# Kernel optimization log

Hardware: AMD Instinct MI355X
Metric: run time of the kernel (lower is better)

## Reference

```python
import jax, jax.numpy as jnp
import numpy as np

B, N, D, H = 4, 2048, 1024, 16
HD = D // H          # head dim before LRPE doubling
CHUNK = 64
BASE = 10000.0
EPS = 1e-6


def setup_inputs() -> dict:
    key = jax.random.key(0)
    ks = jax.random.split(key, 8)
    s = 0.02
    return {
        "x": jax.random.normal(ks[0], (B, N, D), jnp.float32),
        "Wq": jax.random.normal(ks[1], (D, D), jnp.float32) * s,
        "Wk": jax.random.normal(ks[2], (D, D), jnp.float32) * s,
        "Wv": jax.random.normal(ks[3], (D, D), jnp.float32) * s,
        "Wo": jax.random.normal(ks[4], (D, D), jnp.float32) * s,
        "Wg1": jax.random.normal(ks[5], (D, H), jnp.float32) * s,
        "Wg2": jax.random.normal(ks[6], (H, D), jnp.float32) * s,
        "norm_w": jnp.ones((D,), jnp.float32),
    }


def _lrpe(x, theta):
    # cosine LRPE (lrpe_type=6): d -> 2d, concat([x*cos, x*sin])
    c = jnp.cos(theta)[None, :, None, :]
    s = jnp.sin(theta)[None, :, None, :]
    return jnp.concatenate([x * c, x * s], axis=-1)


def _chunk_gla(q, k, v, g):
    # GLA chunked scan: S_t = diag(exp(g_t)) S_{t-1} + k_t^T v_t ; o_t = q_t S_t
    # q,k,g: (b,n,h,dk), v: (b,n,h,dv)
    b, n, h, dk = q.shape
    dv = v.shape[-1]
    nc = n // CHUNK

    def to_chunks(t):
        return t.reshape(b, nc, CHUNK, t.shape[2], t.shape[3]).transpose(1, 0, 2, 3, 4)

    qc, kc, vc, gc = map(to_chunks, (q, k, v, g))  # (nc,b,C,h,*)
    mask = jnp.tril(jnp.ones((CHUNK, CHUNK), bool))

    def step(S, inp):
        qi, ki, vi, gi = inp                      # (b,C,h,dk/dv)
        G = jnp.cumsum(gi, axis=1)                # inclusive cumsum of log decay
        q_g = qi * jnp.exp(G)
        k_g = ki * jnp.exp(-G)
        o_inter = jnp.einsum('bchk,bhkv->bchv', q_g, S)
        A = jnp.einsum('bchk,bshk->bhcs', q_g, k_g)
        A = jnp.where(mask[None, None], A, 0.0)
        o_intra = jnp.einsum('bhcs,bshv->bchv', A, vi)
        G_last = G[:, -1:]                        # (b,1,h,dk)
        S = S * jnp.exp(G_last[:, 0])[..., None] + jnp.einsum(
            'bchk,bchv->bhkv', ki * jnp.exp(G_last - G), vi)
        return S, o_inter + o_intra

    S0 = jnp.zeros((b, h, dk, dv), q.dtype)
    _, o = jax.lax.scan(step, S0, (qc, kc, vc, gc))
    return o.transpose(1, 0, 2, 3, 4).reshape(b, n, h, dv)


def reference(x, Wq, Wk, Wv, Wo, Wg1, Wg2, norm_w):
    b, n, d = x.shape
    q = jax.nn.silu(x @ Wq).reshape(b, n, H, HD)
    k_raw = (x @ Wk).reshape(b, n, H, HD)
    v = (x @ Wv).reshape(b, n, H, HD)

    # log-space cumulative decay from raw k projection (scalar_decay=False path)
    f = jnp.concatenate([jnp.zeros((b, 1, H, HD), jnp.float32),
                         k_raw.astype(jnp.float32)], axis=1)
    z = jax.lax.cumlogsumexp(f, axis=1)           # (b,n+1,H,HD)
    log_f = z[:, :-1] - z[:, 1:]                  # per-step log decay (<=0)
    k = jnp.exp(k_raw - z[:, 1:])                 # normalized keys

    # cosine LRPE: angles (n,HD), doubles head dim
    theta = jnp.arange(n, dtype=jnp.float32)[:, None] * \
        (BASE ** (-2.0 * jnp.arange(HD, dtype=jnp.float32) / HD))[None]
    q = _lrpe(q, theta)
    k = _lrpe(k, theta)
    g = jnp.concatenate([log_f, log_f], axis=-1)  # repeat '... d -> ... (2 d)'

    o = _chunk_gla(q, k, v, g)                    # (b,n,H,HD)
    o = o.reshape(b, n, d)

    gate = jax.nn.sigmoid((x @ Wg1) @ Wg2)        # low-rank output gate
    o = o * gate
    o = o * jax.lax.rsqrt(jnp.mean(o * o, axis=-1, keepdims=True) + EPS) * norm_w
    return o @ Wo
```

## Files before the change

### kernel.cpp

```cpp
#include <hip/hip_runtime.h>
#include <hip/hip_bf16.h>
#include <math.h>

#define B_ 4
#define N_ 2048
#define D_ 1024
#define H_ 16
#define HD_ 64

typedef __attribute__((ext_vector_type(8))) short bf16x8;
typedef __attribute__((ext_vector_type(8))) unsigned short u16x8;
typedef __attribute__((ext_vector_type(4))) float f32x4;

#define AS1(p) ((const __attribute__((address_space(1))) void*)(p))
#define AS3(p) ((__attribute__((address_space(3))) void*)(p))

__device__ inline float bf2f(unsigned short u) { return __uint_as_float(((unsigned)u) << 16); }
__device__ inline unsigned short f2bf(float f) {
  unsigned u = __float_as_uint(f);
  return (unsigned short)((u + 0x7fffu + ((u >> 16) & 1u)) >> 16);
}
__device__ inline unsigned short f2h(float f) {
  _Float16 h = (_Float16)f; unsigned short u; __builtin_memcpy(&u, &h, 2); return u;
}
__device__ inline float h2f(unsigned short u) {
  _Float16 h; __builtin_memcpy(&h, &u, 2); return (float)h;
}
__device__ inline float lseop_fast(float a, float b) {
  float mx = fmaxf(a, b), mn = fminf(a, b);
  return mx + __logf(1.f + __expf(mn - mx));
}

__global__ __launch_bounds__(256) void prep_all(
    const float* __restrict__ x, const float* __restrict__ Wq,
    const float* __restrict__ Wk, const float* __restrict__ Wv,
    const float* __restrict__ Wo, const float* __restrict__ Wg1,
    unsigned short* __restrict__ xb, unsigned short* __restrict__ Wqkv_p,
    unsigned short* __restrict__ Wo_p, unsigned short* __restrict__ Wg1p,
    float* __restrict__ ropeT) {
  const int bid = blockIdx.x;
  if (bid < 4096) {
    const int t = bid * 256 + threadIdx.x;
    float4 a = ((const float4*)x)[(size_t)t * 2];
    float4 b = ((const float4*)x)[(size_t)t * 2 + 1];
    union { unsigned short u[8]; uint4 q; } pk;
    pk.u[0] = f2bf(a.x); pk.u[1] = f2bf(a.y); pk.u[2] = f2bf(a.z); pk.u[3] = f2bf(a.w);
    pk.u[4] = f2bf(b.x); pk.u[5] = f2bf(b.y); pk.u[6] = f2bf(b.z); pk.u[7] = f2bf(b.w);
    ((uint4*)xb)[t] = pk.q;
  } else if (bid < 6144) {
    const int wb = bid - 4096;
    const int which = wb >> 9;
    const float* W = (which == 0) ? Wq : (which == 1) ? Wk : (which == 2) ? Wv : Wo;
    const int col0 = (which == 1) ? 1024 : (which == 2) ? 2048 : 0;
    const int Ntot = (which == 3) ? 1024 : 3072;
    unsigned short* dst = (which == 3) ? Wo_p : Wqkv_p;
    const int t = (wb & 511) * 256 + threadIdx.x;
    const int kg = t >> 10, n = t & 1023;
    union { unsigned short u[8]; uint4 q; } pk;
#pragma unroll
    for (int r = 0; r < 8; ++r)
      pk.u[r] = f2bf(W[(size_t)(kg * 8 + r) * 1024 + n]);
    *(uint4*)&dst[((size_t)kg * Ntot + col0 + n) * 8] = pk.q;
  } else if (bid < 6656) {
    const int t = (bid - 6144) * 256 + threadIdx.x;
    const int n = t >> 6, hd = t & 63;
    const float freq = expf((float)hd * -0.28782313662425575f);
    float s, c;
    sincosf((float)n * freq, &s, &c);
    ropeT[(size_t)n * 128 + hd] = c;
    ropeT[(size_t)n * 128 + 64 + hd] = s;
  } else {
    const int t = (bid - 6656) * 256 + threadIdx.x;
    const int kg = t >> 4, hh = t & 15;
    union { unsigned short us[8]; u16x8 v; } pk;
#pragma unroll
    for (int r = 0; r < 8; ++r)
      pk.us[r] = f2bf(Wg1[(size_t)(kg * 8 + r) * 16 + hh]);
    *(u16x8*)&Wg1p[((size_t)kg * 16 + hh) * 8] = pk.v;
  }
}

__global__ __launch_bounds__(256) void gate_logits(
    const unsigned short* __restrict__ x_bf, const unsigned short* __restrict__ Wg1p,
    float* __restrict__ tg) {
  __shared__ unsigned short Wl[128 * 16 * 8];
  const int tid = threadIdx.x;
  const int lane = tid & 63, w = tid >> 6;
  const int lr = lane & 15, lg = lane >> 4;
#pragma unroll
  for (int u = 0; u < 8; ++u) {
    const int flat = u * 256 + tid;
    *(u16x8*)&Wl[flat * 8] = *(const u16x8*)&Wg1p[(size_t)flat * 8];
  }
  __syncthreads();
  const int row = blockIdx.x * 64 + w * 16 + lr;
  f32x4 acc = (f32x4){0.f, 0.f, 0.f, 0.f};
  for (int ks = 0; ks < 32; ++ks) {
    bf16x8 a = *(const bf16x8*)&x_bf[(size_t)row * 1024 + ks * 32 + lg * 8];
    bf16x8 b = *(const bf16x8*)&Wl[((ks * 4 + lg) * 16 + lr) * 8];
    acc = __builtin_amdgcn_mfma_f32_16x16x32_bf16(a, b, acc, 0, 0, 0);
  }
  const int orow = blockIdx.x * 64 + w * 16 + 4 * lg;
#pragma unroll
  for (int reg = 0; reg < 4; ++reg)
    tg[(size_t)(orow + reg) * 16 + lr] = acc[reg];
}

__global__ __launch_bounds__(256) void gemm_qkv(
    const unsigned short* __restrict__ A, const unsigned short* __restrict__ Wp,
    unsigned short* __restrict__ qb, unsigned short* __restrict__ keh,
    unsigned short* __restrict__ vb, float* __restrict__ T, int M, int K) {
  const int Nn = 3072;
  __shared__ unsigned short Asm[2][128 * 32];
  __shared__ unsigned short Bsm[2][4 * 128 * 8];

  const int tid = threadIdx.x;
  const int lane = tid & 63;
  const int w = tid >> 6;
  const int nwg = gridDim.x;
  const int cpx = nwg >> 3;
  const int orig = blockIdx.x;
  const int L = (orig & 7) * cpx + (orig >> 3);
  const int st = L >> 6;
  const int j = L & 63;
  const int by = (st / 3) * 8 + (j >> 3);
  const int bx = (st % 3) * 8 + (j & 7);
  const int m0 = by * 128, n0 = bx * 128;
  const int wr = w >> 1, wc = w & 1;

  f32x4 acc[4][4];
#pragma unroll
  for (int i = 0; i < 4; ++i)
#pragma unroll
    for (int jj = 0; jj < 4; ++jj) acc[i][jj] = (f32x4){0.f, 0.f, 0.f, 0.f};

  const int rA0 = w * 16 + (lane >> 2);
  const int rA1 = (w + 4) * 16 + (lane >> 2);
  const int sA0 = (lane & 3) ^ ((rA0 >> 1) & 3);
  const int sA1 = (lane & 3) ^ ((rA1 >> 1) & 3);
  const unsigned short* gA0 = A + (size_t)(m0 + rA0) * K + sA0 * 8;
  const unsigned short* gA1 = A + (size_t)(m0 + rA1) * K + sA1 * 8;
  const unsigned short* gB0 = Wp + (size_t)(w >> 1) * Nn * 8 +
                              (size_t)(n0 + (w & 1) * 64 + lane) * 8;
  const unsigned short* gB1 = Wp + (size_t)((w + 4) >> 1) * Nn * 8 +
                              (size_t)(n0 + ((w + 4) & 1) * 64 + lane) * 8;

  int offA[4], offB[4];
#pragma unroll
  for (int m = 0; m < 4; ++m) {
    const int rowf = wr * 64 + m * 16 + (lane & 15);
    const int sp = (lane >> 4) ^ ((rowf >> 1) & 3);
    offA[m] = rowf * 32 + sp * 8;
  }
#pragma unroll
  for (int n = 0; n < 4; ++n) {
    const int colf = wc * 64 + n * 16 + (lane & 15);
    offB[n] = (lane >> 4) * 1024 + colf * 8;
  }

  auto STAGE = [&](int buf, int t) {
    const int kt = t * 32;
    const size_t kB = (size_t)(kt >> 3) * Nn * 8;
    __builtin_amdgcn_global_load_lds(AS1(gA0 + kt), AS3(&Asm[buf][w * 512]), 16, 0, 0);
    __builtin_amdgcn_global_load_lds(AS1(gA1 + kt), AS3(&Asm[buf][(w + 4) * 512]), 16, 0, 0);
    __builtin_amdgcn_global_load_lds(AS1(gB0 + kB), AS3(&Bsm[buf][w * 512]), 16, 0, 0);
    __builtin_amdgcn_global_load_lds(AS1(gB1 + kB), AS3(&Bsm[buf][(w + 4) * 512]), 16, 0, 0);
  };

  const int NT = K >> 5;
  STAGE(0, 0);
  __syncthreads();
  int cur = 0;
  for (int t = 0; t < NT; ++t) {
    if (t + 1 < NT) STAGE(cur ^ 1, t + 1);
    bf16x8 af[4], bfr[4];
#pragma unroll
    for (int m = 0; m < 4; ++m) af[m] = *(const bf16x8*)&Asm[cur][offA[m]];
#pragma unroll
    for (int n = 0; n < 4; ++n) bfr[n] = *(const bf16x8*)&Bsm[cur][offB[n]];
#pragma unroll
    for (int m = 0; m < 4; ++m)
#pragma unroll
      for (int n = 0; n < 4; ++n)
        acc[m][n] = __builtin_amdgcn_mfma_f32_16x16x32_bf16(af[m], bfr[n], acc[m][n], 0, 0, 0);
    __syncthreads();
    cur ^= 1;
  }

  const int crow = (lane >> 4) * 4;
  const int ccol = lane & 15;
  const int slice = bx >> 3;
  if (slice == 1) {
#pragma unroll
    for (int n = 0; n < 4; ++n) {
      float se = 0.f;
#pragma unroll
      for (int m = 0; m < 4; ++m)
#pragma unroll
        for (int r = 0; r < 4; ++r) {
          float ev = __expf(acc[m][n][r]);
          se += ev;
          keh[(size_t)(m0 + wr * 64 + m * 16 + crow + r) * 1024 +
              (n0 & 1023) + wc * 64 + n * 16 + ccol] = f2h(ev);
        }
      se += __shfl_xor(se, 16);
      se += __shfl_xor(se, 32);
      if ((lane >> 4) == 0) {
        const int bb = m0 >> 11;
        const int h = ((n0 & 1023) + wc * 64) >> 6;
        const int hd = n * 16 + ccol;
        const int c = ((m0 & 2047) >> 6) + wr;
        T[(size_t)((bb * 16 + h) * 64 + hd) * 32 + c] = __logf(se);
      }
    }
  } else {
#pragma unroll
    for (int m = 0; m < 4; ++m)
#pragma unroll
      for (int n = 0; n < 4; ++n)
#pragma unroll
        for (int r = 0; r < 4; ++r) {
          float vv = acc[m][n][r];
          const size_t idx = (size_t)(m0 + wr * 64 + m * 16 + crow + r) * 1024 +
                             (n0 & 1023) + wc * 64 + n * 16 + ccol;
          if (slice == 0) {
            vv = vv / (1.f + __expf(-vv));
            qb[idx] = f2bf(vv);
          } else {
            vb[idx] = f2bf(vv);
          }
        }
  }
}

__global__ __launch_bounds__(256) void gemm_bf16(
    const unsigned short* __restrict__ A, const unsigned short* __restrict__ Wp,
    float* __restrict__ Cf, int M, int K, int Nn) {
  __shared__ unsigned short Asm[2][128 * 32];
  __shared__ unsigned short Bsm[2][4 * 128 * 8];

  const int tid = threadIdx.x;
  const int lane = tid & 63;
  const int w = tid >> 6;
  const int nb = Nn >> 7;
  const int nwg = gridDim.x;
  const int cpx = nwg >> 3;
  int bid = blockIdx.x;
  bid = (bid & 7) * cpx + (bid >> 3);
  const int by = bid / nb, bx = bid % nb;
  const int m0 = by * 128, n0 = bx * 128;
  const int wr = w >> 1, wc = w & 1;

  f32x4 acc[4][4];
#pragma unroll
  for (int i = 0; i < 4; ++i)
#pragma unroll
    for (int j = 0; j < 4; ++j) acc[i][j] = (f32x4){0.f, 0.f, 0.f, 0.f};

  const int rA0 = w * 16 + (lane >> 2);
  const int rA1 = (w + 4) * 16 + (lane >> 2);
  const int sA0 = (lane & 3) ^ ((rA0 >> 1) & 3);
  const int sA1 = (lane & 3) ^ ((rA1 >> 1) & 3);
  const unsigned short* gA0 = A + (size_t)(m0 + rA0) * K + sA0 * 8;
  const unsigned short* gA1 = A + (size_t)(m0 + rA1) * K + sA1 * 8;
  const unsigned short* gB0 = Wp + (size_t)(w >> 1) * Nn * 8 +
                              (size_t)(n0 + (w & 1) * 64 + lane) * 8;
  const unsigned short* gB1 = Wp + (size_t)((w + 4) >> 1) * Nn * 8 +
                              (size_t)(n0 + ((w + 4) & 1) * 64 + lane) * 8;

  int offA[4], offB[4];
#pragma unroll
  for (int m = 0; m < 4; ++m) {
    const int rowf = wr * 64 + m * 16 + (lane & 15);
    const int sp = (lane >> 4) ^ ((rowf >> 1) & 3);
    offA[m] = rowf * 32 + sp * 8;
  }
#pragma unroll
  for (int n = 0; n < 4; ++n) {
    const int colf = wc * 64 + n * 16 + (lane & 15);
    offB[n] = (lane >> 4) * 1024 + colf * 8;
  }

  auto STAGE = [&](int buf, int t) {
    const int kt = t * 32;
    const size_t kB = (size_t)(kt >> 3) * Nn * 8;
    __builtin_amdgcn_global_load_lds(AS1(gA0 + kt), AS3(&Asm[buf][w * 512]), 16, 0, 0);
    __builtin_amdgcn_global_load_lds(AS1(gA1 + kt), AS3(&Asm[buf][(w + 4) * 512]), 16, 0, 0);
    __builtin_amdgcn_global_load_lds(AS1(gB0 + kB), AS3(&Bsm[buf][w * 512]), 16, 0, 0);
    __builtin_amdgcn_global_load_lds(AS1(gB1 + kB), AS3(&Bsm[buf][(w + 4) * 512]), 16, 0, 0);
  };

  const int NT = K >> 5;
  STAGE(0, 0);
  __syncthreads();
  int cur = 0;
  for (int t = 0; t < NT; ++t) {
    if (t + 1 < NT) STAGE(cur ^ 1, t + 1);
    bf16x8 af[4], bfr[4];
#pragma unroll
    for (int m = 0; m < 4; ++m) af[m] = *(const bf16x8*)&Asm[cur][offA[m]];
#pragma unroll
    for (int n = 0; n < 4; ++n) bfr[n] = *(const bf16x8*)&Bsm[cur][offB[n]];
#pragma unroll
    for (int m = 0; m < 4; ++m)
#pragma unroll
      for (int n = 0; n < 4; ++n)
        acc[m][n] = __builtin_amdgcn_mfma_f32_16x16x32_bf16(af[m], bfr[n], acc[m][n], 0, 0, 0);
    __syncthreads();
    cur ^= 1;
  }

  const int crow = (lane >> 4) * 4;
  const int ccol = lane & 15;
#pragma unroll
  for (int m = 0; m < 4; ++m)
#pragma unroll
    for (int n = 0; n < 4; ++n) {
#pragma unroll
      for (int r = 0; r < 4; ++r) {
        Cf[(size_t)(m0 + wr * 64 + m * 16 + crow + r) * Nn +
           n0 + wc * 64 + n * 16 + ccol] = acc[m][n][r];
      }
    }
}

__global__ void scan_pass_b(const float* __restrict__ T, float* __restrict__ Pf) {
  const int ch = blockIdx.x * 256 + threadIdx.x;
  const float* t = &T[(size_t)ch * 32];
  float* p = &Pf[(size_t)ch * 32];
  float run = 0.f;
  for (int c = 0; c < 32; ++c) {
    p[c] = run;
    run = lseop_fast(run, t[c]);
  }
}

__global__ __launch_bounds__(256) void gla_a(
    const unsigned short* __restrict__ qs, const unsigned short* __restrict__ keh,
    const float* __restrict__ Pf, const unsigned short* __restrict__ v_bf,
    const float* __restrict__ ropeT,
    unsigned short* __restrict__ qg_p, unsigned short* __restrict__ U,
    unsigned short* __restrict__ o_bf, float* __restrict__ glast_g) {
  __shared__ unsigned short kg_l[64 * 128];
  __shared__ unsigned short kgT_l[128 * 72];
  __shared__ unsigned short vT_l[64 * 72];
  __shared__ unsigned short G_l[64 * 72];
  __shared__ unsigned short tot_l[4][64];
  __shared__ float glast_s[64];
  unsigned short* A_l = G_l;

  const int bid = blockIdx.x;
  const int bh = bid >> 5, c = bid & 31;
  const int b = bh >> 4, h = bh & 15;
  const int t0 = c * 64;
  const int tid = threadIdx.x;
  const int lane = tid & 63, w = tid >> 6;
  const int lr = lane & 15, lg = lane >> 4;

  const size_t qv_base = ((size_t)(b * N_ + t0) * H_ + h) * 64;

  const int jch = tid & 63, qq = tid >> 6;
  float e[16];
  {
    const float escale = __expf(-Pf[((size_t)bh * 64 + jch) * 32 + c]);
    float psum = 0.f;
#pragma unroll
    for (int i = 0; i < 16; ++i) {
      const int r = qq * 16 + i;
      float ei = h2f(keh[qv_base + (size_t)r * 1024 + jch]) * escale;
      e[i] = ei;
      psum += ei;
      float cv = ropeT[(size_t)(t0 + r) * 128 + jch];
      float sv = ropeT[(size_t)(t0 + r) * 128 + 64 + jch];
      kg_l[r * 128 + (((jch >> 3) ^ (r & 7)) << 3) + (jch & 7)] = f2bf(ei * cv);
      kg_l[r * 128 + ((((jch + 64) >> 3) ^ (r & 7)) << 3) + (jch & 7)] = f2bf(ei * sv);
    }
    tot_l[qq][jch] = f2h(psum);
  }
  {
    const int r = tid >> 2, d0 = (tid & 3) * 16;
    u16x8 a = *(const u16x8*)&v_bf[qv_base + (size_t)r * (H_ * 64) + d0];
    u16x8 b2 = *(const u16x8*)&v_bf[qv_base + (size_t)r * (H_ * 64) + d0 + 8];
#pragma unroll
    for (int ee = 0; ee < 8; ++ee) {
      vT_l[(d0 + ee) * 72 + r] = a[ee];
      vT_l[(d0 + 8 + ee) * 72 + r] = b2[ee];
    }
  }
  __syncthreads();
  {
    float off = 0.f;
    for (int p = 0; p < qq; ++p) off += h2f(tot_l[p][jch]);
    float S = off;
#pragma unroll
    for (int i = 0; i < 16; ++i) {
      S += e[i];
      G_l[(qq * 16 + i) * 72 + jch] = f2h(-__logf(1.f + S));
    }
    if (qq == 3) {
      glast_g[(size_t)bid * 64 + jch] = -__logf(1.f + S);
      glast_s[jch] = 1.f / (1.f + S);
    }
  }
  {
    const int j = tid >> 1, sh = (tid & 1) * 32;
#pragma unroll
    for (int u = 0; u < 4; ++u) {
      union { unsigned short us[8]; u16x8 v; } tv;
#pragma unroll
      for (int ee = 0; ee < 8; ++ee) {
        const int s = sh + 8 * u + ee;
        tv.us[ee] = kg_l[s * 128 + (((j >> 3) ^ (s & 7)) * 8) + (j & 7)];
      }
      *(u16x8*)&kgT_l[j * 72 + sh + 8 * u] = tv.v;
    }
  }
  __syncthreads();

  bf16x8 af[4];
  {
    const int r = 16 * w + lr;
#pragma unroll
    for (int ks = 0; ks < 4; ++ks) {
      const int jb = 32 * ks + 8 * lg;
      const int jq = jb & 63;
      u16x8 q8 = *(const u16x8*)&qs[qv_base + (size_t)r * (H_ * 64) + jq];
      u16x8 gh8 = *(const u16x8*)&G_l[r * 72 + jq];
      float4 r0 = *(const float4*)&ropeT[(size_t)(t0 + r) * 128 + jb];
      float4 r1 = *(const float4*)&ropeT[(size_t)(t0 + r) * 128 + jb + 4];
      float rr[8] = {r0.x, r0.y, r0.z, r0.w, r1.x, r1.y, r1.z, r1.w};
      union { unsigned short us[8]; bf16x8 v; u16x8 uv; } pk;
#pragma unroll
      for (int ee = 0; ee < 8; ++ee)
        pk.us[ee] = f2bf(bf2f(q8[ee]) * rr[ee] * __expf(h2f(gh8[ee])));
      af[ks] = pk.v;
      *(u16x8*)&qg_p[((((size_t)bid * 4 + w) * 4 + ks) * 64 + lane) * 8] = pk.uv;
    }
  }
  f32x4 acc1[4];
#pragma unroll
  for (int n = 0; n < 4; ++n) acc1[n] = (f32x4){0.f, 0.f, 0.f, 0.f};
#pragma unroll
  for (int n = 0; n < 4; ++n) {
    const int s = 16 * n + lr;
#pragma unroll
    for (int ks = 0; ks < 4; ++ks) {
      bf16x8 bk = *(const bf16x8*)&kg_l[s * 128 + (((lg + 4 * ks) ^ (s & 7)) * 8)];
      acc1[n] = __builtin_amdgcn_mfma_f32_16x16x32_bf16(af[ks], bk, acc1[n], 0, 0, 0);
    }
  }
  __syncthreads();
#pragma unroll
  for (int n = 0; n < 4; ++n) {
    const int s = 16 * n + lr;
#pragma unroll
    for (int reg = 0; reg < 4; ++reg) {
      const int cr = 16 * w + 4 * lg + reg;
      A_l[cr * 72 + s] = (s <= cr) ? f2bf(acc1[n][reg]) : (unsigned short)0;
    }
  }
  f32x4 acc2[8];
#pragma unroll
  for (int n = 0; n < 8; ++n) acc2[n] = (f32x4){0.f, 0.f, 0.f, 0.f};
#pragma unroll
  for (int ks = 0; ks < 2; ++ks) {
    const int s0 = 32 * ks + 8 * lg;
    bf16x8 av = *(const bf16x8*)&vT_l[(16 * w + lr) * 72 + s0];
#pragma unroll
    for (int n = 0; n < 8; ++n) {
      bf16x8 bk = *(const bf16x8*)&kgT_l[(16 * n + lr) * 72 + s0];
      acc2[n] = __builtin_amdgcn_mfma_f32_16x16x32_bf16(av, bk, acc2[n], 0, 0, 0);
    }
  }
  __syncthreads();
  float es[4];
#pragma unroll
  for (int n = 0; n < 4; ++n) es[n] = glast_s[16 * n + lr];
#pragma unroll
  for (int n = 0; n < 8; ++n) {
    const int j = 16 * n + lr;
    const float ee = es[n & 3];
#pragma unroll
    for (int reg = 0; reg < 4; ++reg)
      kg_l[(16 * w + 4 * lg + reg) * 128 + j] = f2bf(acc2[n][reg] * ee);
  }
  f32x4 acc3[4];
#pragma unroll
  for (int n = 0; n < 4; ++n) acc3[n] = (f32x4){0.f, 0.f, 0.f, 0.f};
#pragma unroll
  for (int ks = 0; ks < 2; ++ks) {
    const int s0 = 32 * ks + 8 * lg;
    bf16x8 aA = *(const bf16x8*)&A_l[(16 * w + lr) * 72 + s0];
#pragma unroll
    for (int n = 0; n < 4; ++n) {
      bf16x8 bV = *(const bf16x8*)&vT_l[(16 * n + lr) * 72 + s0];
      acc3[n] = __builtin_amdgcn_mfma_f32_16x16x32_bf16(aA, bV, acc3[n], 0, 0, 0);
    }
  }
#pragma unroll
  for (int n = 0; n < 4; ++n)
#pragma unroll
    for (int reg = 0; reg < 4; ++reg)
      o_bf[qv_base + (size_t)(16 * w + 4 * lg + reg) * (H_ * 64) + 16 * n + lr] =
          f2bf(acc3[n][reg]);
  __syncthreads();
#pragma unroll
  for (int u = 0; u < 4; ++u) {
    const int flat = u * 256 + tid;
    const int d = flat >> 4, sl = flat & 15;
    *(u16x8*)&U[((size_t)bid * 64 + d) * 128 + sl * 8] =
        *(const u16x8*)&kg_l[d * 128 + sl * 8];
  }
}

__global__ __launch_bounds__(256) void gla_b(unsigned short* __restrict__ U,
                                             const float* __restrict__ glast_g) {
  const int t = blockIdx.x * 256 + threadIdx.x;
  const int j4 = t & 31;
  const int d = (t >> 5) & 63;
  const int bh = t >> 11;
  const int jj0 = (4 * j4) & 63;
  float s0 = 0.f, s1 = 0.f, s2 = 0.f, s3 = 0.f;
  for (int c = 0; c < 32; ++c) {
    const size_t ub = ((size_t)((bh * 32 + c) * 64 + d)) * 128 + 4 * j4;
    ushort4 uv = *(const ushort4*)&U[ub];
    float4 g4 = *(const float4*)&glast_g[(size_t)(bh * 32 + c) * 64 + jj0];
    ushort4 pv;
    pv.x = f2bf(s0); pv.y = f2bf(s1); pv.z = f2bf(s2); pv.w = f2bf(s3);
    *(ushort4*)&U[ub] = pv;
    s0 = s0 * __expf(g4.x) + bf2f(uv.x);
    s1 = s1 * __expf(g4.y) + bf2f(uv.y);
    s2 = s2 * __expf(g4.z) + bf2f(uv.z);
    s3 = s3 * __expf(g4.w) + bf2f(uv.w);
  }
}

__global__ __launch_bounds__(256) void gla_c(
    const unsigned short* __restrict__ qg_p, const unsigned short* __restrict__ S,
    unsigned short* __restrict__ o_bf) {
  __shared__ unsigned short S_l[64 * 128];
  const int bid = blockIdx.x;
  const int bh = bid >> 5, c = bid & 31;
  const int b = bh >> 4, h = bh & 15;
  const int t0 = c * 64;
  const int tid = threadIdx.x;
  const int lane = tid & 63, w = tid >> 6;
  const int lr = lane & 15, lg = lane >> 4;
  const size_t s_base = (size_t)bid * 64 * 128;
  const size_t o_base = ((size_t)(b * N_ + t0) * H_ + h) * 64;

#pragma unroll
  for (int u = 0; u < 4; ++u) {
    const int flat = u * 256 + tid;
    const int d = flat >> 4, sl = flat & 15;
    u16x8 src = *(const u16x8*)&S[s_base + (size_t)d * 128 + sl * 8];
    *(u16x8*)&S_l[d * 128 + ((sl ^ (d & 7)) * 8)] = src;
  }
  __syncthreads();
  bf16x8 af[4];
#pragma unroll
  for (int ks = 0; ks < 4; ++ks)
    af[ks] = *(const bf16x8*)&qg_p[((((size_t)bid * 4 + w) * 4 + ks) * 64 + lane) * 8];
  f32x4 acc[4];
#pragma unroll
  for (int n = 0; n < 4; ++n) acc[n] = (f32x4){0.f, 0.f, 0.f, 0.f};
#pragma unroll
  for (int n = 0; n < 4; ++n) {
    const int d = 16 * n + lr;
#pragma unroll
    for (int ks = 0; ks < 4; ++ks) {
      bf16x8 bk = *(const bf16x8*)&S_l[d * 128 + (((lg + 4 * ks) ^ (d & 7)) * 8)];
      acc[n] = __builtin_amdgcn_mfma_f32_16x16x32_bf16(af[ks], bk, acc[n], 0, 0, 0);
    }
  }
#pragma unroll
  for (int n = 0; n < 4; ++n)
#pragma unroll
    for (int reg = 0; reg < 4; ++reg) {
      const size_t idx = o_base + (size_t)(16 * w + 4 * lg + reg) * (H_ * 64) + 16 * n + lr;
      o_bf[idx] = f2bf(bf2f(o_bf[idx]) + acc[n][reg]);
    }
}

__global__ __launch_bounds__(256) void gate_norm2(
    const float* __restrict__ tg, const float* __restrict__ Wg2,
    const float* __restrict__ nw, const unsigned short* __restrict__ o_bf,
    unsigned short* __restrict__ og) {
  const int w = threadIdx.x >> 6, lane = threadIdx.x & 63;
  const int row = blockIdx.x * 4 + w;
  float tgv[16];
  const float* tp = &tg[(size_t)row * 16];
#pragma unroll
  for (int hh = 0; hh < 16; ++hh) tgv[hh] = tp[hh];
  float ogr[4][4];
  float ssq = 0.f;
#pragma unroll
  for (int u = 0; u < 4; ++u) {
    const int d0 = u * 256 + lane * 4;
    ushort4 o4 = *(const ushort4*)&o_bf[(size_t)row * 1024 + d0];
    float oa[4] = {bf2f(o4.x), bf2f(o4.y), bf2f(o4.z), bf2f(o4.w)};
    float sgx = 0.f, sgy = 0.f, sgz = 0.f, sgw = 0.f;
#pragma unroll
    for (int hh = 0; hh < 16; ++hh) {
      float4 w4 = *(const float4*)&Wg2[hh * 1024 + d0];
      sgx += tgv[hh] * w4.x; sgy += tgv[hh] * w4.y;
      sgz += tgv[hh] * w4.z; sgw += tgv[hh] * w4.w;
    }
    ogr[u][0] = oa[0] / (1.f + __expf(-sgx));
    ogr[u][1] = oa[1] / (1.f + __expf(-sgy));
    ogr[u][2] = oa[2] / (1.f + __expf(-sgz));
    ogr[u][3] = oa[3] / (1.f + __expf(-sgw));
    ssq += ogr[u][0] * ogr[u][0] + ogr[u][1] * ogr[u][1] +
           ogr[u][2] * ogr[u][2] + ogr[u][3] * ogr[u][3];
  }
#pragma unroll
  for (int off = 32; off > 0; off >>= 1) ssq += __shfl_xor(ssq, off);
  const float rinv = rsqrtf(ssq * (1.f / 1024.f) + 1e-6f);
#pragma unroll
  for (int u = 0; u < 4; ++u) {
    const int d0 = u * 256 + lane * 4;
    float4 nw4 = *(const float4*)&nw[d0];
    ushort4 st;
    st.x = f2bf(ogr[u][0] * rinv * nw4.x);
    st.y = f2bf(ogr[u][1] * rinv * nw4.y);
    st.z = f2bf(ogr[u][2] * rinv * nw4.z);
    st.w = f2bf(ogr[u][3] * rinv * nw4.w);
    *(ushort4*)&og[(size_t)row * 1024 + d0] = st;
  }
}

extern "C" void kernel_launch(void* const* d_in, const int* in_sizes, int n_in,
                              void* d_out, int out_size, void* d_ws, size_t ws_size,
                              hipStream_t stream) {
  const float* x   = (const float*)d_in[0];
  const float* Wq  = (const float*)d_in[1];
  const float* Wk  = (const float*)d_in[2];
  const float* Wv  = (const float*)d_in[3];
  const float* Wo  = (const float*)d_in[4];
  const float* Wg1 = (const float*)d_in[5];
  const float* Wg2 = (const float*)d_in[6];
  const float* nw  = (const float*)d_in[7];
  float* out = (float*)d_out;
  float* ws  = (float*)d_ws;

  const size_t P = (size_t)B_ * N_ * D_;
  unsigned short* keh = (unsigned short*)ws;
  unsigned short* o_bf = (unsigned short*)(ws + P);
  unsigned short* qg_p = (unsigned short*)(ws + 3 * P);
  unsigned short* U_buf = (unsigned short*)(ws + 4 * P);
  unsigned short* v_bf = (unsigned short*)(ws + 5 * P);
  unsigned short* q_bf = (unsigned short*)(ws + 5 * P + P / 2);
  float* ropeT = ws + 6 * P;
  float* T_buf = ws + 6 * P + 524288;
  float* P_buf = T_buf + 131072;
  unsigned short* Wg1p = (unsigned short*)(ws + 6 * P + 786432);
  float* tg_buf = ws + 6 * P + 794624;
  unsigned short* x_bf = (unsigned short*)(ws + 13 * P / 2);
  unsigned short* og_bf = x_bf;
  unsigned short* Wqkv_p = (unsigned short*)(ws + 7 * P);
  unsigned short* Wo_p = (unsigned short*)(ws + 7 * P + 1572864);
  float* glast_g = ws + 7 * P + 2097152;

  const int M = B_ * N_;
  const int ggrid = (M / 128) * (D_ / 128);
  const int qkvgrid = (M / 128) * (3 * D_ / 128);

  prep_all<<<6664, 256, 0, stream>>>(x, Wq, Wk, Wv, Wo, Wg1,
                                     x_bf, Wqkv_p, Wo_p, Wg1p, ropeT);
  gate_logits<<<M / 64, 256, 0, stream>>>(x_bf, Wg1p, tg_buf);
  gemm_qkv<<<qkvgrid, 256, 0, stream>>>(x_bf, Wqkv_p, q_bf, keh, v_bf, T_buf, M, D_);
  scan_pass_b<<<16, 256, 0, stream>>>(T_buf, P_buf);
  gla_a<<<2048, 256, 0, stream>>>(q_bf, keh, P_buf, v_bf, ropeT, qg_p, U_buf, o_bf, glast_g);
  gla_b<<<512, 256, 0, stream>>>(U_buf, glast_g);
  gla_c<<<2048, 256, 0, stream>>>(qg_p, U_buf, o_bf);
  gate_norm2<<<M / 4, 256, 0, stream>>>(tg_buf, Wg2, nw, o_bf, og_bf);
  gemm_bf16<<<ggrid, 256, 0, stream>>>(og_bf, Wo_p, out, M, D_, D_);
}
```

Baseline: 207.2 us.

## Fold gate logits into QKV GEMM grid and inline chunk prefix scan

The gate-logit MFMA work now runs as extra workgroups appended to the QKV GEMM launch, reusing its shared memory in two halves, so one kernel launch goes away. The separate cross-chunk log-sum-exp scan kernel is also removed. Each gla_a block instead recomputes its own prefix from the per-chunk totals with up to 31 sequential lseop steps per thread. This trades two launches and one buffer round trip for redundant serial work in gla_a and some tail imbalance in the GEMM grid.

```diff
diff --git a/kernel.cpp b/kernel.cpp
--- a/kernel.cpp
+++ b/kernel.cpp
@@ -80,46 +80,52 @@
   }
 }
 
-__global__ __launch_bounds__(256) void gate_logits(
-    const unsigned short* __restrict__ x_bf, const unsigned short* __restrict__ Wg1p,
-    float* __restrict__ tg) {
-  __shared__ unsigned short Wl[128 * 16 * 8];
-  const int tid = threadIdx.x;
-  const int lane = tid & 63, w = tid >> 6;
-  const int lr = lane & 15, lg = lane >> 4;
-#pragma unroll
-  for (int u = 0; u < 8; ++u) {
-    const int flat = u * 256 + tid;
-    *(u16x8*)&Wl[flat * 8] = *(const u16x8*)&Wg1p[(size_t)flat * 8];
-  }
-  __syncthreads();
-  const int row = blockIdx.x * 64 + w * 16 + lr;
-  f32x4 acc = (f32x4){0.f, 0.f, 0.f, 0.f};
-  for (int ks = 0; ks < 32; ++ks) {
-    bf16x8 a = *(const bf16x8*)&x_bf[(size_t)row * 1024 + ks * 32 + lg * 8];
-    bf16x8 b = *(const bf16x8*)&Wl[((ks * 4 + lg) * 16 + lr) * 8];
-    acc = __builtin_amdgcn_mfma_f32_16x16x32_bf16(a, b, acc, 0, 0, 0);
-  }
-  const int orow = blockIdx.x * 64 + w * 16 + 4 * lg;
-#pragma unroll
-  for (int reg = 0; reg < 4; ++reg)
-    tg[(size_t)(orow + reg) * 16 + lr] = acc[reg];
-}
-
 __global__ __launch_bounds__(256) void gemm_qkv(
     const unsigned short* __restrict__ A, const unsigned short* __restrict__ Wp,
     unsigned short* __restrict__ qb, unsigned short* __restrict__ keh,
-    unsigned short* __restrict__ vb, float* __restrict__ T, int M, int K) {
+    unsigned short* __restrict__ vb, float* __restrict__ T,
+    const unsigned short* __restrict__ Wg1p, float* __restrict__ tg,
+    int M, int K) {
   const int Nn = 3072;
+  const int NWG_MAIN = 1536;
   __shared__ unsigned short Asm[2][128 * 32];
   __shared__ unsigned short Bsm[2][4 * 128 * 8];
 
   const int tid = threadIdx.x;
   const int lane = tid & 63;
   const int w = tid >> 6;
-  const int nwg = gridDim.x;
-  const int cpx = nwg >> 3;
+  const int lr = lane & 15, lg = lane >> 4;
   const int orig = blockIdx.x;
+
+  if (orig >= NWG_MAIN) {
+    const int gb = orig - NWG_MAIN;
+    unsigned short* Wl = &Asm[0][0];
+    f32x4 acc = (f32x4){0.f, 0.f, 0.f, 0.f};
+    const int row = gb * 64 + w * 16 + lr;
+#pragma unroll
+    for (int half = 0; half < 2; ++half) {
+      __syncthreads();
+#pragma unroll
+      for (int u = 0; u < 4; ++u) {
+        const int flat = u * 256 + tid;
+        *(u16x8*)&Wl[flat * 8] = *(const u16x8*)&Wg1p[(size_t)(half * 8192 + flat * 8)];
+      }
+      __syncthreads();
+      for (int ks2 = 0; ks2 < 16; ++ks2) {
+        const int ks = half * 16 + ks2;
+        bf16x8 a = *(const bf16x8*)&A[(size_t)row * 1024 + ks * 32 + lg * 8];
+        bf16x8 b = *(const bf16x8*)&Wl[((ks2 * 4 + lg) * 16 + lr) * 8];
+        acc = __builtin_amdgcn_mfma_f32_16x16x32_bf16(a, b, acc, 0, 0, 0);
+      }
+    }
+    const int orow = gb * 64 + w * 16 + 4 * lg;
+#pragma unroll
+    for (int reg = 0; reg < 4; ++reg)
+      tg[(size_t)(orow + reg) * 16 + lr] = acc[reg];
+    return;
+  }
+
+  const int cpx = NWG_MAIN >> 3;
   const int L = (orig & 7) * cpx + (orig >> 3);
   const int st = L >> 6;
   const int j = L & 63;
@@ -324,20 +330,9 @@
     }
 }
 
-__global__ void scan_pass_b(const float* __restrict__ T, float* __restrict__ Pf) {
-  const int ch = blockIdx.x * 256 + threadIdx.x;
-  const float* t = &T[(size_t)ch * 32];
-  float* p = &Pf[(size_t)ch * 32];
-  float run = 0.f;
-  for (int c = 0; c < 32; ++c) {
-    p[c] = run;
-    run = lseop_fast(run, t[c]);
-  }
-}
-
 __global__ __launch_bounds__(256) void gla_a(
     const unsigned short* __restrict__ qs, const unsigned short* __restrict__ keh,
-    const float* __restrict__ Pf, const unsigned short* __restrict__ v_bf,
+    const float* __restrict__ T, const unsigned short* __restrict__ v_bf,
     const float* __restrict__ ropeT,
     unsigned short* __restrict__ qg_p, unsigned short* __restrict__ U,
     unsigned short* __restrict__ o_bf, float* __restrict__ glast_g) {
@@ -362,7 +357,10 @@
   const int jch = tid & 63, qq = tid >> 6;
   float e[16];
   {
-    const float escale = __expf(-Pf[((size_t)bh * 64 + jch) * 32 + c]);
+    const float* trow = &T[((size_t)bh * 64 + jch) * 32];
+    float Pv = 0.f;
+    for (int cc = 0; cc < c; ++cc) Pv = lseop_fast(Pv, trow[cc]);
+    const float escale = __expf(-Pv);
     float psum = 0.f;
 #pragma unroll
     for (int i = 0; i < 16; ++i) {
@@ -652,7 +650,6 @@
   unsigned short* q_bf = (unsigned short*)(ws + 5 * P + P / 2);
   float* ropeT = ws + 6 * P;
   float* T_buf = ws + 6 * P + 524288;
-  float* P_buf = T_buf + 131072;
   unsigned short* Wg1p = (unsigned short*)(ws + 6 * P + 786432);
   float* tg_buf = ws + 6 * P + 794624;
   unsigned short* x_bf = (unsigned short*)(ws + 13 * P / 2);
@@ -663,14 +660,13 @@
 
   const int M = B_ * N_;
   const int ggrid = (M / 128) * (D_ / 128);
-  const int qkvgrid = (M / 128) * (3 * D_ / 128);
+  const int qkvgrid = (M / 128) * (3 * D_ / 128) + M / 64;
 
   prep_all<<<6664, 256, 0, stream>>>(x, Wq, Wk, Wv, Wo, Wg1,
                                      x_bf, Wqkv_p, Wo_p, Wg1p, ropeT);
-  gate_logits<<<M / 64, 256, 0, stream>>>(x_bf, Wg1p, tg_buf);
-  gemm_qkv<<<qkvgrid, 256, 0, stream>>>(x_bf, Wqkv_p, q_bf, keh, v_bf, T_buf, M, D_);
-  scan_pass_b<<<16, 256, 0, stream>>>(T_buf, P_buf);
-  gla_a<<<2048, 256, 0, stream>>>(q_bf, keh, P_buf, v_bf, ropeT, qg_p, U_buf, o_bf, glast_g);
+  gemm_qkv<<<qkvgrid, 256, 0, stream>>>(x_bf, Wqkv_p, q_bf, keh, v_bf, T_buf,
+                                        Wg1p, tg_buf, M, D_);
+  gla_a<<<2048, 256, 0, stream>>>(q_bf, keh, T_buf, v_bf, ropeT, qg_p, U_buf, o_bf, glast_g);
   gla_b<<<512, 256, 0, stream>>>(U_buf, glast_g);
   gla_c<<<2048, 256, 0, stream>>>(qg_p, U_buf, o_bf);
   gate_norm2<<<M / 4, 256, 0, stream>>>(tg_buf, Wg2, nw, o_bf, og_bf);
```

After: 239.9 us. 15.8% more time.
